# Kernel tuning notes

Measured on AMD Instinct MI355X. Metric: run time of the kernel, lower is better.

## Reference

```python
import jax, jax.numpy as jnp
import numpy as np

H = 32          # query heads
D = 128         # head_dim
THETA = 10000.0
NEG = -1e30


def _rope_cos_sin(positions, d):
    half = d // 2
    inv_freq = 1.0 / (THETA ** (jnp.arange(0, d, 2, dtype=jnp.float32) / d))  # [half]
    ang = positions.astype(jnp.float32)[:, None] * inv_freq[None, :]          # [B, half]
    return jnp.cos(ang), jnp.sin(ang)


def _apply_rope(x, cos, sin):
    # neox-style rotary on last dim; cos/sin broadcast over leading dims
    half = x.shape[-1] // 2
    x1, x2 = x[..., :half], x[..., half:]
    return jnp.concatenate([x1 * cos - x2 * sin, x2 * cos + x1 * sin], axis=-1)


def setup_inputs() -> dict:
    key = jax.random.key(0)
    ks = jax.random.split(key, 8)
    B, hidden = 64, 4096
    num_blocks, block_size, max_blocks = 16384, 16, 256
    hidden_states = jax.random.normal(ks[0], (B, hidden), dtype=jnp.float32)
    wqkv = jax.random.normal(ks[1], (hidden, (H + 2) * D), dtype=jnp.float32) * 0.02
    wdense = jax.random.normal(ks[2], (hidden, hidden), dtype=jnp.float32) * 0.02
    k_cache = jax.random.normal(ks[3], (num_blocks, block_size, D), dtype=jnp.float32)
    v_cache = jax.random.normal(ks[4], (num_blocks, block_size, D), dtype=jnp.float32)
    # each sequence owns a distinct set of 256 blocks
    block_tables = jnp.arange(B * max_blocks, dtype=jnp.int64).reshape(B, max_blocks)
    context_lens = jax.random.randint(ks[5], (B,), 1, max_blocks * block_size + 1).astype(jnp.int64)
    positions = context_lens - 1  # position of the new (current) token
    return {
        "hidden_states": hidden_states, "wqkv": wqkv, "wdense": wdense,
        "k_cache": k_cache, "v_cache": v_cache,
        "positions": positions, "block_tables": block_tables,
        "context_lens": context_lens,
    }


def reference(hidden_states, wqkv, wdense, k_cache, v_cache,
              positions, block_tables, context_lens):
    B = hidden_states.shape[0]
    block_size = k_cache.shape[1]
    scale = 1.0 / np.sqrt(D).astype(np.float32)

    # fused QKV projection (bias=False in Falcon-7B config)
    qkv = hidden_states @ wqkv                                  # [B,(H+2)*D]
    q = qkv[:, : H * D].reshape(B, H, D)
    k = qkv[:, H * D : (H + 1) * D]                             # [B,D]  (MQA, 1 kv head)
    v = qkv[:, (H + 1) * D :]                                   # [B,D]

    # rotary embedding on q and k at the current positions
    cos, sin = _rope_cos_sin(positions, D)                      # [B,D/2]
    q = _apply_rope(q, cos[:, None, :], sin[:, None, :])
    k = _apply_rope(k, cos, sin)

    # write the new token's k/v into the paged cache (scatter)
    rows = jnp.arange(B)
    blk = block_tables[rows, positions // block_size]           # [B]
    off = positions % block_size
    k_cache = k_cache.at[blk, off].set(k)
    v_cache = v_cache.at[blk, off].set(v)

    # paged gather: assemble each sequence's KV from its block table
    keys = k_cache[block_tables].reshape(B, -1, D)              # [B,L,D]
    vals = v_cache[block_tables].reshape(B, -1, D)
    L = keys.shape[1]

    scores = jnp.einsum('bhd,bld->bhl', q, keys) * scale        # [B,H,L]
    valid = jnp.arange(L)[None, :] < context_lens[:, None]      # [B,L]
    scores = jnp.where(valid[:, None, :], scores, NEG)
    probs = jax.nn.softmax(scores, axis=-1)
    attn = jnp.einsum('bhl,bld->bhd', probs, vals).reshape(B, H * D)

    return attn @ wdense                                        # [B,hidden]
```

## Files before the change

kernel.cpp:

```cpp
#include <hip/hip_runtime.h>
#include <hip/hip_bf16.h>
#include <cmath>

#define NHEADS 32
#define DIM 128
#define SPLITS 32
#define WIN 128
#define TILE 32
#define KSPLIT 16
#define QKV_N 4352
#define HID 4096

typedef __attribute__((ext_vector_type(4))) float f32x4;
typedef __attribute__((ext_vector_type(8))) short short8i;
typedef __attribute__((ext_vector_type(4))) short short4i;

__device__ __forceinline__ unsigned short f2bf(float x) {
  __hip_bfloat16 h = __float2bfloat16(x);
  return *reinterpret_cast<unsigned short*>(&h);
}
__device__ __forceinline__ unsigned int pk2bf(float lo, float hi) {
  return (unsigned)f2bf(lo) | ((unsigned)f2bf(hi) << 16);
}
__device__ __forceinline__ float bf2f(unsigned short u) {
  unsigned int b = ((unsigned int)u) << 16;
  return __uint_as_float(b);
}

__device__ __forceinline__ f32x4 mfma16bf16(short4i a, short4i b, f32x4 c) {
#if __has_builtin(__builtin_amdgcn_mfma_f32_16x16x16bf16_1k)
  return __builtin_amdgcn_mfma_f32_16x16x16bf16_1k(a, b, c, 0, 0, 0);
#else
  asm volatile("v_mfma_f32_16x16x16_bf16 %0, %1, %2, %0"
               : "+v"(c) : "v"(a), "v"(b));
  return c;
#endif
}

__global__ __launch_bounds__(256, 4) void gemm64_mfma(
    const float* __restrict__ A, const float* __restrict__ W,
    float* __restrict__ P, int N, int K)
{
  __shared__ unsigned short Ab[64][40];
  __shared__ unsigned short Wt[64][40];
  const int t = threadIdx.x;
  const int w = t >> 6, lane = t & 63;
  const int l4 = lane >> 4, l16 = lane & 15;
  const int n0 = blockIdx.x * 64;
  const int KS = K / KSPLIT;
  const int kbase = blockIdx.y * KS;

  const int ar = t >> 2, akq = t & 3;
  const int bn = t & 63, bkq = t >> 6;

  f32x4 acc[4];
#pragma unroll
  for (int i = 0; i < 4; ++i) acc[i] = (f32x4){0.f, 0.f, 0.f, 0.f};

  float4 a0, a1;
  float bw[8];

#define GLOAD(KC)                                                          \
  {                                                                        \
    const float* ap = A + (size_t)ar * K + kbase + (KC) + akq * 8;         \
    a0 = *(const float4*)ap;                                               \
    a1 = *(const float4*)(ap + 4);                                         \
    const float* wp = W + (size_t)(kbase + (KC) + bkq * 8) * N + n0 + bn;  \
    _Pragma("unroll")                                                      \
    for (int j = 0; j < 8; ++j) bw[j] = wp[(size_t)j * N];                 \
  }

#define SWRITE                                                             \
  {                                                                        \
    unsigned int ua[4] = {pk2bf(a0.x, a0.y), pk2bf(a0.z, a0.w),            \
                          pk2bf(a1.x, a1.y), pk2bf(a1.z, a1.w)};           \
    *(float4*)&Ab[ar][akq * 8] = *(float4*)ua;                             \
    unsigned int ub[4] = {pk2bf(bw[0], bw[1]), pk2bf(bw[2], bw[3]),        \
                          pk2bf(bw[4], bw[5]), pk2bf(bw[6], bw[7])};       \
    *(float4*)&Wt[bn][bkq * 8] = *(float4*)ub;                             \
  }

  GLOAD(0);
  SWRITE;
  __syncthreads();

  for (int kc = 0; kc < KS; kc += 32) {
    const bool pre = (kc + 32 < KS);
    if (pre) GLOAD(kc + 32);

    const short8i af = *(const short8i*)&Ab[w * 16 + l16][l4 * 8];
#pragma unroll
    for (int nt = 0; nt < 4; ++nt) {
      const short8i bf = *(const short8i*)&Wt[nt * 16 + l16][l4 * 8];
      acc[nt] = __builtin_amdgcn_mfma_f32_16x16x32_bf16(af, bf, acc[nt], 0, 0, 0);
    }

    __syncthreads();
    if (pre) {
      SWRITE;
      __syncthreads();
    }
  }

  float* base = P + (size_t)blockIdx.y * 64 * N + n0;
#pragma unroll
  for (int nt = 0; nt < 4; ++nt)
#pragma unroll
    for (int r = 0; r < 4; ++r)
      base[(size_t)(w * 16 + l4 * 4 + r) * N + nt * 16 + l16] = acc[nt][r];
#undef GLOAD
#undef SWRITE
}

__global__ __launch_bounds__(256) void reduce_parts(
    const float* __restrict__ P, float* __restrict__ C, int total)
{
  const int i = (blockIdx.x * 256 + threadIdx.x) * 4;
  if (i >= total) return;
  float4 s = *(const float4*)(P + i);
#pragma unroll
  for (int k = 1; k < KSPLIT; ++k) {
    const float4 v = *(const float4*)(P + (size_t)k * total + i);
    s.x += v.x; s.y += v.y; s.z += v.z; s.w += v.w;
  }
  *(float4*)(C + i) = s;
}

__global__ __launch_bounds__(256) void rope_kernel(
    float* __restrict__ qkv, const int* __restrict__ positions)
{
  const int b = blockIdx.x;
  float* row = qkv + (size_t)b * QKV_N;
  const float pos = (float)positions[b];
  for (int it = threadIdx.x; it < 33 * 64; it += 256) {
    const int r = it >> 6, i = it & 63;
    float* x = row + (r < 32 ? r * DIM : HID);
    const float ex = (float)(2 * i) * (1.0f / 128.0f);
    const float inv = 1.0f / powf(10000.0f, ex);
    const float ang = pos * inv;
    const float c = cosf(ang), sn = sinf(ang);
    const float x1 = x[i], x2 = x[i + 64];
    x[i]      = x1 * c - x2 * sn;
    x[i + 64] = x2 * c + x1 * sn;
  }
}

__global__ __launch_bounds__(256, 4) void attn_kernel(
    const float* __restrict__ qkv,
    const float* __restrict__ k_cache, const float* __restrict__ v_cache,
    const int* __restrict__ block_tables, const int* __restrict__ context_lens,
    float* __restrict__ pl, unsigned short* __restrict__ pacc)
{
  const int b = blockIdx.x, s = blockIdx.y;
  const int ctx = context_lens[b];
  const int start = s * WIN;
  if (start >= ctx) return;
  const int end = min(start + WIN, ctx);
  const int pos = ctx - 1;
  const int nt = (end - start + TILE - 1) / TILE;

  const int t = threadIdx.x;
  const int w = t >> 6, lane = t & 63;
  const int hq = w >> 1, pq = w & 1;
  const int l4 = lane >> 4, l16 = lane & 15;

  __shared__ unsigned short KbU[32 * 128];
  __shared__ unsigned short VtU[128 * 34];
  __shared__ float red[2][64][36];
  __shared__ int bt_lds[8];

  const float* qbase = qkv + (size_t)b * QKV_N;
  const int bt0 = start >> 4;
  if (t < 8) {
    const int idx = bt0 + t;
    bt_lds[t] = (idx < 256) ? block_tables[b * 256 + idx] : 0;
  }

  const float scale = 0.08838834764831845f;
  short8i qf[4];
  {
    const float* qp0 = qbase + (hq * 16 + l16) * DIM + l4 * 8;
#pragma unroll
    for (int ks = 0; ks < 4; ++ks) {
      const float4 a = *(const float4*)(qp0 + ks * 32);
      const float4 c = *(const float4*)(qp0 + ks * 32 + 4);
      union { unsigned int u[4]; short8i v; } qc;
      qc.u[0] = pk2bf(a.x * scale, a.y * scale);
      qc.u[1] = pk2bf(a.z * scale, a.w * scale);
      qc.u[2] = pk2bf(c.x * scale, c.y * scale);
      qc.u[3] = pk2bf(c.z * scale, c.w * scale);
      qf[ks] = qc.v;
    }
  }

  f32x4 o2[8];
#pragma unroll
  for (int i = 0; i < 8; ++i) o2[i] = (f32x4){0.f, 0.f, 0.f, 0.f};
  float lh = 0.f;

  float4 kreg[4], vreg[4];
  const int tk_sub = t >> 5;
  const int tk_col = t & 31;

#define LOADREGS(T0)                                                     \
  {                                                                      \
    _Pragma("unroll")                                                    \
    for (int j = 0; j < 4; ++j) {                                        \
      int gp_ = (T0) + j * 8 + tk_sub;                                   \
      if (gp_ > pos) gp_ = pos;                                          \
      const float* kp;                                                   \
      if (gp_ == pos) kp = qbase + HID;                                  \
      else {                                                             \
        const int blk = bt_lds[(gp_ >> 4) - bt0];                        \
        kp = k_cache + ((size_t)blk * 16 + (gp_ & 15)) * DIM;            \
      }                                                                  \
      kreg[j] = *(const float4*)(kp + tk_col * 4);                       \
    }                                                                    \
    int gv = (T0) + tk_col;                                              \
    if (gv > pos) gv = pos;                                              \
    const float* vp;                                                     \
    if (gv == pos) vp = qbase + HID + DIM;                               \
    else {                                                               \
      const int blk = bt_lds[(gv >> 4) - bt0];                           \
      vp = v_cache + ((size_t)blk * 16 + (gv & 15)) * DIM;               \
    }                                                                    \
    _Pragma("unroll")                                                    \
    for (int j = 0; j < 4; ++j)                                          \
      vreg[j] = *(const float4*)(vp + tk_sub * 16 + j * 4);              \
  }

#define WRITE_TILE                                                                     \
  {                                                                                    \
    _Pragma("unroll")                                                                  \
    for (int j = 0; j < 4; ++j) {                                                      \
      const int pl_ = j * 8 + tk_sub;                                                  \
      const int up = (tk_col >> 1) ^ (pl_ & 15);                                       \
      unsigned int lo = pk2bf(kreg[j].x, kreg[j].y);                                   \
      unsigned int hi = pk2bf(kreg[j].z, kreg[j].w);                                   \
      unsigned int* dst = (unsigned int*)&KbU[pl_ * 128 + up * 8 + (tk_col & 1) * 4];  \
      dst[0] = lo; dst[1] = hi;                                                        \
    }                                                                                  \
    _Pragma("unroll")                                                                  \
    for (int j = 0; j < 4; ++j) {                                                      \
      const int od0 = tk_sub * 16 + j * 4;                                             \
      VtU[(od0 + 0) * 34 + tk_col] = f2bf(vreg[j].x);                                  \
      VtU[(od0 + 1) * 34 + tk_col] = f2bf(vreg[j].y);                                  \
      VtU[(od0 + 2) * 34 + tk_col] = f2bf(vreg[j].z);                                  \
      VtU[(od0 + 3) * 34 + tk_col] = f2bf(vreg[j].w);                                  \
    }                                                                                  \
  }

  __syncthreads();
  LOADREGS(start);
  WRITE_TILE;
  __syncthreads();

  for (int it = 0; it < nt; ++it) {
    const int t0 = start + it * TILE;
    const bool pre = (it + 1 < nt);
    if (pre) LOADREGS(t0 + TILE);

    f32x4 accs = {0.f, 0.f, 0.f, 0.f};
    const int rowK = pq * 16 + l16;
#pragma unroll
    for (int ks = 0; ks < 4; ++ks) {
      const int up = (l4 + ks * 4) ^ l16;
      const short8i kf = *(const short8i*)&KbU[rowK * 128 + up * 8];
      accs = __builtin_amdgcn_mfma_f32_16x16x32_bf16(kf, qf[ks], accs, 0, 0, 0);
    }

    const int pb_ = t0 + pq * 16 + l4 * 4;
    const float p0 = (pb_ + 0 < end) ? __expf(accs[0]) : 0.f;
    const float p1 = (pb_ + 1 < end) ? __expf(accs[1]) : 0.f;
    const float p2 = (pb_ + 2 < end) ? __expf(accs[2]) : 0.f;
    const float p3 = (pb_ + 3 < end) ? __expf(accs[3]) : 0.f;
    lh += (p0 + p1) + (p2 + p3);
    union { unsigned int u[2]; short4i v; } pc;
    pc.u[0] = pk2bf(p0, p1);
    pc.u[1] = pk2bf(p2, p3);
    const short4i pf = pc.v;

    const int vb = pq * 16 + l4 * 4;
#pragma unroll
    for (int ob = 0; ob < 8; ++ob) {
      const int rowV = ob * 16 + l16;
      union { unsigned int u[2]; short4i v; } vc;
      vc.u[0] = *(const unsigned int*)&VtU[rowV * 34 + vb];
      vc.u[1] = *(const unsigned int*)&VtU[rowV * 34 + vb + 2];
      o2[ob] = mfma16bf16(pf, vc.v, o2[ob]);
    }

    if (pre) {
      __syncthreads();
      WRITE_TILE;
      __syncthreads();
    }
  }

  float lhr = lh;
  lhr += __shfl_xor(lhr, 16);
  lhr += __shfl_xor(lhr, 32);

  if (pq == 1) {
#pragma unroll
    for (int ob = 0; ob < 8; ++ob) *(f32x4*)&red[hq][lane][ob * 4] = o2[ob];
    red[hq][lane][32] = lhr;
  }
  __syncthreads();
  if (pq == 0) {
#pragma unroll
    for (int ob = 0; ob < 8; ++ob) {
      const f32x4 r4 = *(const f32x4*)&red[hq][lane][ob * 4];
      o2[ob] += r4;
    }
    lhr += red[hq][lane][32];
    const size_t sbase = (size_t)(b * SPLITS + s) * NHEADS + hq * 16;
#pragma unroll
    for (int ob = 0; ob < 8; ++ob) {
      pacc[(sbase + l4 * 4 + 0) * DIM + ob * 16 + l16] = f2bf(o2[ob][0]);
      pacc[(sbase + l4 * 4 + 1) * DIM + ob * 16 + l16] = f2bf(o2[ob][1]);
      pacc[(sbase + l4 * 4 + 2) * DIM + ob * 16 + l16] = f2bf(o2[ob][2]);
      pacc[(sbase + l4 * 4 + 3) * DIM + ob * 16 + l16] = f2bf(o2[ob][3]);
    }
    if (lane < 16) pl[sbase + lane] = lhr;
  }
#undef LOADREGS
#undef WRITE_TILE
}

__global__ __launch_bounds__(128) void combine_kernel(
    const float* __restrict__ pl, const unsigned short* __restrict__ pacc,
    const int* __restrict__ context_lens, float* __restrict__ attn)
{
  const int bh = blockIdx.x;
  const int b = bh >> 5, h = bh & 31;
  const int d = threadIdx.x;
  const int ctx = context_lens[b];
  const int ns = (ctx + WIN - 1) / WIN;
  float L = 0.f, o = 0.f;
  for (int s = 0; s < ns; ++s) {
    const size_t idx = (size_t)(b * SPLITS + s) * NHEADS + h;
    L += pl[idx];
    o += bf2f(pacc[idx * DIM + d]);
  }
  attn[(size_t)b * HID + h * DIM + d] = o / L;
}

extern "C" void kernel_launch(void* const* d_in, const int* in_sizes, int n_in,
                              void* d_out, int out_size, void* d_ws, size_t ws_size,
                              hipStream_t stream) {
  const float* hidden   = (const float*)d_in[0];
  const float* wqkv     = (const float*)d_in[1];
  const float* wdense   = (const float*)d_in[2];
  const float* k_cache  = (const float*)d_in[3];
  const float* v_cache  = (const float*)d_in[4];
  const int* positions    = (const int*)d_in[5];
  const int* block_tables = (const int*)d_in[6];
  const int* context_lens = (const int*)d_in[7];
  float* out = (float*)d_out;

  float* qkv  = (float*)d_ws;
  float* attn = qkv + 64 * QKV_N;
  float* un   = attn + 64 * HID;
  float* gp   = un;
  unsigned short* pacc = (unsigned short*)un;
  float* pl   = un + (size_t)64 * SPLITS * NHEADS * DIM / 2;

  gemm64_mfma<<<dim3(QKV_N / 64, KSPLIT), 256, 0, stream>>>(hidden, wqkv, gp, QKV_N, HID);
  reduce_parts<<<(64 * QKV_N) / 1024, 256, 0, stream>>>(gp, qkv, 64 * QKV_N);
  rope_kernel<<<64, 256, 0, stream>>>(qkv, positions);
  attn_kernel<<<dim3(64, SPLITS), 256, 0, stream>>>(qkv, k_cache, v_cache,
                                                    block_tables, context_lens, pl, pacc);
  combine_kernel<<<64 * NHEADS, 128, 0, stream>>>(pl, pacc, context_lens, attn);
  gemm64_mfma<<<dim3(HID / 64, KSPLIT), 256, 0, stream>>>(attn, wdense, gp, HID, HID);
  reduce_parts<<<(64 * HID) / 1024, 256, 0, stream>>>(gp, out, 64 * HID);
}
```

Baseline: 109.8 us.

## Balance attention splits by context length and drop intra-block head-pair reduction

Replaces fixed 128-token windows with per-sequence equal chunks across 16 splits, so every block does similar work. Each block now uses two waves (one per 16-head group) that cover all 32 tile rows themselves, removing the LDS reduction between wave pairs. V is stored row-major in LDS with both K and V loaded per token row. The combine kernel always sums all splits. Fewer threads per block and scalar 16-bit LDS reads for V fragments may reduce latency hiding and add LDS traffic.

```diff
diff --git a/kernel.cpp b/kernel.cpp
--- a/kernel.cpp
+++ b/kernel.cpp
@@ -4,12 +4,12 @@
 
 #define NHEADS 32
 #define DIM 128
-#define SPLITS 32
-#define WIN 128
+#define SPLITS 16
 #define TILE 32
 #define KSPLIT 16
 #define QKV_N 4352
 #define HID 4096
+#define VSTR 132
 
 typedef __attribute__((ext_vector_type(4))) float f32x4;
 typedef __attribute__((ext_vector_type(8))) short short8i;
@@ -145,37 +145,35 @@
   }
 }
 
-__global__ __launch_bounds__(256, 4) void attn_kernel(
+__global__ __launch_bounds__(128, 3) void attn_kernel(
     const float* __restrict__ qkv,
     const float* __restrict__ k_cache, const float* __restrict__ v_cache,
     const int* __restrict__ block_tables, const int* __restrict__ context_lens,
     float* __restrict__ pl, unsigned short* __restrict__ pacc)
 {
   const int b = blockIdx.x, s = blockIdx.y;
-  const int ctx = context_lens[b];
-  const int start = s * WIN;
-  if (start >= ctx) return;
-  const int end = min(start + WIN, ctx);
-  const int pos = ctx - 1;
-  const int nt = (end - start + TILE - 1) / TILE;
-
   const int t = threadIdx.x;
   const int w = t >> 6, lane = t & 63;
-  const int hq = w >> 1, pq = w & 1;
   const int l4 = lane >> 4, l16 = lane & 15;
+  const int ctx = context_lens[b];
+  const int pos = ctx - 1;
+  const int chunk = (ctx + SPLITS - 1) / SPLITS;
+  const int start = s * chunk;
+  const int end = min(start + chunk, ctx);
+  const int nt = (end > start) ? ((end - start + TILE - 1) / TILE) : 0;
 
   __shared__ unsigned short KbU[32 * 128];
-  __shared__ unsigned short VtU[128 * 34];
-  __shared__ float red[2][64][36];
-  __shared__ int bt_lds[8];
+  __shared__ unsigned short VL[TILE][VSTR];
+  __shared__ int bt_lds[20];
 
   const float* qbase = qkv + (size_t)b * QKV_N;
   const int bt0 = start >> 4;
-  if (t < 8) {
+  if (t < 20) {
     const int idx = bt0 + t;
     bt_lds[t] = (idx < 256) ? block_tables[b * 256 + idx] : 0;
   }
 
+  const int hq = w;
   const float scale = 0.08838834764831845f;
   short8i qf[4];
   {
@@ -198,102 +196,94 @@
   for (int i = 0; i < 8; ++i) o2[i] = (f32x4){0.f, 0.f, 0.f, 0.f};
   float lh = 0.f;
 
-  float4 kreg[4], vreg[4];
-  const int tk_sub = t >> 5;
-  const int tk_col = t & 31;
+  const int tcol = t & 31;
+  const int tsub = t >> 5;
+  float4 kreg[8], vreg[8];
 
 #define LOADREGS(T0)                                                     \
   {                                                                      \
     _Pragma("unroll")                                                    \
-    for (int j = 0; j < 4; ++j) {                                        \
-      int gp_ = (T0) + j * 8 + tk_sub;                                   \
+    for (int j = 0; j < 8; ++j) {                                        \
+      int gp_ = (T0) + j * 4 + tsub;                                     \
       if (gp_ > pos) gp_ = pos;                                          \
-      const float* kp;                                                   \
-      if (gp_ == pos) kp = qbase + HID;                                  \
+      const float *kp, *vp;                                              \
+      if (gp_ == pos) { kp = qbase + HID; vp = qbase + HID + DIM; }      \
       else {                                                             \
         const int blk = bt_lds[(gp_ >> 4) - bt0];                        \
-        kp = k_cache + ((size_t)blk * 16 + (gp_ & 15)) * DIM;            \
+        const size_t cidx = ((size_t)blk * 16 + (gp_ & 15)) * DIM;       \
+        kp = k_cache + cidx; vp = v_cache + cidx;                        \
       }                                                                  \
-      kreg[j] = *(const float4*)(kp + tk_col * 4);                       \
+      kreg[j] = ((const float4*)kp)[tcol];                               \
+      vreg[j] = ((const float4*)vp)[tcol];                               \
     }                                                                    \
-    int gv = (T0) + tk_col;                                              \
-    if (gv > pos) gv = pos;                                              \
-    const float* vp;                                                     \
-    if (gv == pos) vp = qbase + HID + DIM;                               \
-    else {                                                               \
-      const int blk = bt_lds[(gv >> 4) - bt0];                           \
-      vp = v_cache + ((size_t)blk * 16 + (gv & 15)) * DIM;               \
-    }                                                                    \
-    _Pragma("unroll")                                                    \
-    for (int j = 0; j < 4; ++j)                                          \
-      vreg[j] = *(const float4*)(vp + tk_sub * 16 + j * 4);              \
-  }
-
-#define WRITE_TILE                                                                     \
-  {                                                                                    \
-    _Pragma("unroll")                                                                  \
-    for (int j = 0; j < 4; ++j) {                                                      \
-      const int pl_ = j * 8 + tk_sub;                                                  \
-      const int up = (tk_col >> 1) ^ (pl_ & 15);                                       \
-      unsigned int lo = pk2bf(kreg[j].x, kreg[j].y);                                   \
-      unsigned int hi = pk2bf(kreg[j].z, kreg[j].w);                                   \
-      unsigned int* dst = (unsigned int*)&KbU[pl_ * 128 + up * 8 + (tk_col & 1) * 4];  \
-      dst[0] = lo; dst[1] = hi;                                                        \
-    }                                                                                  \
-    _Pragma("unroll")                                                                  \
-    for (int j = 0; j < 4; ++j) {                                                      \
-      const int od0 = tk_sub * 16 + j * 4;                                             \
-      VtU[(od0 + 0) * 34 + tk_col] = f2bf(vreg[j].x);                                  \
-      VtU[(od0 + 1) * 34 + tk_col] = f2bf(vreg[j].y);                                  \
-      VtU[(od0 + 2) * 34 + tk_col] = f2bf(vreg[j].z);                                  \
-      VtU[(od0 + 3) * 34 + tk_col] = f2bf(vreg[j].w);                                  \
-    }                                                                                  \
-  }
-
-  __syncthreads();
-  LOADREGS(start);
-  WRITE_TILE;
-  __syncthreads();
-
-  for (int it = 0; it < nt; ++it) {
-    const int t0 = start + it * TILE;
-    const bool pre = (it + 1 < nt);
-    if (pre) LOADREGS(t0 + TILE);
-
-    f32x4 accs = {0.f, 0.f, 0.f, 0.f};
-    const int rowK = pq * 16 + l16;
-#pragma unroll
-    for (int ks = 0; ks < 4; ++ks) {
-      const int up = (l4 + ks * 4) ^ l16;
-      const short8i kf = *(const short8i*)&KbU[rowK * 128 + up * 8];
-      accs = __builtin_amdgcn_mfma_f32_16x16x32_bf16(kf, qf[ks], accs, 0, 0, 0);
-    }
-
-    const int pb_ = t0 + pq * 16 + l4 * 4;
-    const float p0 = (pb_ + 0 < end) ? __expf(accs[0]) : 0.f;
-    const float p1 = (pb_ + 1 < end) ? __expf(accs[1]) : 0.f;
-    const float p2 = (pb_ + 2 < end) ? __expf(accs[2]) : 0.f;
-    const float p3 = (pb_ + 3 < end) ? __expf(accs[3]) : 0.f;
-    lh += (p0 + p1) + (p2 + p3);
-    union { unsigned int u[2]; short4i v; } pc;
-    pc.u[0] = pk2bf(p0, p1);
-    pc.u[1] = pk2bf(p2, p3);
-    const short4i pf = pc.v;
-
-    const int vb = pq * 16 + l4 * 4;
-#pragma unroll
-    for (int ob = 0; ob < 8; ++ob) {
-      const int rowV = ob * 16 + l16;
-      union { unsigned int u[2]; short4i v; } vc;
-      vc.u[0] = *(const unsigned int*)&VtU[rowV * 34 + vb];
-      vc.u[1] = *(const unsigned int*)&VtU[rowV * 34 + vb + 2];
-      o2[ob] = mfma16bf16(pf, vc.v, o2[ob]);
-    }
-
-    if (pre) {
-      __syncthreads();
-      WRITE_TILE;
-      __syncthreads();
+  }
+
+#define WRITE_TILE                                                                  \
+  {                                                                                 \
+    _Pragma("unroll")                                                               \
+    for (int j = 0; j < 8; ++j) {                                                   \
+      const int row = j * 4 + tsub;                                                 \
+      const int up = (tcol >> 1) ^ (row & 15);                                      \
+      unsigned int* kd = (unsigned int*)&KbU[row * 128 + up * 8 + (tcol & 1) * 4];  \
+      kd[0] = pk2bf(kreg[j].x, kreg[j].y);                                          \
+      kd[1] = pk2bf(kreg[j].z, kreg[j].w);                                          \
+      unsigned int* vd = (unsigned int*)&VL[row][tcol * 4];                         \
+      vd[0] = pk2bf(vreg[j].x, vreg[j].y);                                          \
+      vd[1] = pk2bf(vreg[j].z, vreg[j].w);                                          \
+    }                                                                               \
+  }
+
+  if (nt > 0) {
+    __syncthreads();
+    LOADREGS(start);
+    WRITE_TILE;
+    __syncthreads();
+
+    for (int it = 0; it < nt; ++it) {
+      const int t0 = start + it * TILE;
+      const bool pre = (it + 1 < nt);
+      if (pre) LOADREGS(t0 + TILE);
+
+      short4i pf[2];
+#pragma unroll
+      for (int pg = 0; pg < 2; ++pg) {
+        f32x4 accs = {0.f, 0.f, 0.f, 0.f};
+        const int rowK = pg * 16 + l16;
+#pragma unroll
+        for (int ks = 0; ks < 4; ++ks) {
+          const int up = (l4 + ks * 4) ^ l16;
+          const short8i kf = *(const short8i*)&KbU[rowK * 128 + up * 8];
+          accs = __builtin_amdgcn_mfma_f32_16x16x32_bf16(kf, qf[ks], accs, 0, 0, 0);
+        }
+        const int pb_ = t0 + pg * 16 + l4 * 4;
+        const float p0 = (pb_ + 0 < end) ? __expf(accs[0]) : 0.f;
+        const float p1 = (pb_ + 1 < end) ? __expf(accs[1]) : 0.f;
+        const float p2 = (pb_ + 2 < end) ? __expf(accs[2]) : 0.f;
+        const float p3 = (pb_ + 3 < end) ? __expf(accs[3]) : 0.f;
+        lh += (p0 + p1) + (p2 + p3);
+        union { unsigned int u[2]; short4i v; } pc;
+        pc.u[0] = pk2bf(p0, p1);
+        pc.u[1] = pk2bf(p2, p3);
+        pf[pg] = pc.v;
+      }
+
+#pragma unroll
+      for (int ob = 0; ob < 8; ++ob) {
+#pragma unroll
+        for (int pg = 0; pg < 2; ++pg) {
+          union { unsigned short su[4]; short4i v; } vc;
+#pragma unroll
+          for (int j = 0; j < 4; ++j)
+            vc.su[j] = VL[pg * 16 + l4 * 4 + j][ob * 16 + l16];
+          o2[ob] = mfma16bf16(pf[pg], vc.v, o2[ob]);
+        }
+      }
+
+      if (pre) {
+        __syncthreads();
+        WRITE_TILE;
+        __syncthreads();
+      }
     }
   }
 
@@ -301,44 +291,29 @@
   lhr += __shfl_xor(lhr, 16);
   lhr += __shfl_xor(lhr, 32);
 
-  if (pq == 1) {
-#pragma unroll
-    for (int ob = 0; ob < 8; ++ob) *(f32x4*)&red[hq][lane][ob * 4] = o2[ob];
-    red[hq][lane][32] = lhr;
-  }
-  __syncthreads();
-  if (pq == 0) {
-#pragma unroll
-    for (int ob = 0; ob < 8; ++ob) {
-      const f32x4 r4 = *(const f32x4*)&red[hq][lane][ob * 4];
-      o2[ob] += r4;
-    }
-    lhr += red[hq][lane][32];
-    const size_t sbase = (size_t)(b * SPLITS + s) * NHEADS + hq * 16;
-#pragma unroll
-    for (int ob = 0; ob < 8; ++ob) {
-      pacc[(sbase + l4 * 4 + 0) * DIM + ob * 16 + l16] = f2bf(o2[ob][0]);
-      pacc[(sbase + l4 * 4 + 1) * DIM + ob * 16 + l16] = f2bf(o2[ob][1]);
-      pacc[(sbase + l4 * 4 + 2) * DIM + ob * 16 + l16] = f2bf(o2[ob][2]);
-      pacc[(sbase + l4 * 4 + 3) * DIM + ob * 16 + l16] = f2bf(o2[ob][3]);
-    }
-    if (lane < 16) pl[sbase + lane] = lhr;
-  }
+  const size_t sbase = (size_t)(b * SPLITS + s) * NHEADS + hq * 16;
+#pragma unroll
+  for (int ob = 0; ob < 8; ++ob) {
+    pacc[(sbase + l4 * 4 + 0) * DIM + ob * 16 + l16] = f2bf(o2[ob][0]);
+    pacc[(sbase + l4 * 4 + 1) * DIM + ob * 16 + l16] = f2bf(o2[ob][1]);
+    pacc[(sbase + l4 * 4 + 2) * DIM + ob * 16 + l16] = f2bf(o2[ob][2]);
+    pacc[(sbase + l4 * 4 + 3) * DIM + ob * 16 + l16] = f2bf(o2[ob][3]);
+  }
+  if (lane < 16) pl[sbase + lane] = lhr;
 #undef LOADREGS
 #undef WRITE_TILE
 }
 
 __global__ __launch_bounds__(128) void combine_kernel(
     const float* __restrict__ pl, const unsigned short* __restrict__ pacc,
-    const int* __restrict__ context_lens, float* __restrict__ attn)
+    float* __restrict__ attn)
 {
   const int bh = blockIdx.x;
   const int b = bh >> 5, h = bh & 31;
   const int d = threadIdx.x;
-  const int ctx = context_lens[b];
-  const int ns = (ctx + WIN - 1) / WIN;
   float L = 0.f, o = 0.f;
-  for (int s = 0; s < ns; ++s) {
+#pragma unroll
+  for (int s = 0; s < SPLITS; ++s) {
     const size_t idx = (size_t)(b * SPLITS + s) * NHEADS + h;
     L += pl[idx];
     o += bf2f(pacc[idx * DIM + d]);
@@ -369,9 +344,9 @@
   gemm64_mfma<<<dim3(QKV_N / 64, KSPLIT), 256, 0, stream>>>(hidden, wqkv, gp, QKV_N, HID);
   reduce_parts<<<(64 * QKV_N) / 1024, 256, 0, stream>>>(gp, qkv, 64 * QKV_N);
   rope_kernel<<<64, 256, 0, stream>>>(qkv, positions);
-  attn_kernel<<<dim3(64, SPLITS), 256, 0, stream>>>(qkv, k_cache, v_cache,
+  attn_kernel<<<dim3(64, SPLITS), 128, 0, stream>>>(qkv, k_cache, v_cache,
                                                     block_tables, context_lens, pl, pacc);
-  combine_kernel<<<64 * NHEADS, 128, 0, stream>>>(pl, pacc, context_lens, attn);
+  combine_kernel<<<64 * NHEADS, 128, 0, stream>>>(pl, pacc, attn);
   gemm64_mfma<<<dim3(HID / 64, KSPLIT), 256, 0, stream>>>(attn, wdense, gp, HID, HID);
   reduce_parts<<<(64 * HID) / 1024, 256, 0, stream>>>(gp, out, 64 * HID);
 }
```

Measured after the change: 206.7 us. +88.2%, slower.

## Balance attention splits per sequence, double-buffer LDS tiles, drop in-block reduction

Applied to the files above, without the earlier changes.

Replaces fixed 128-token windows with a per-sequence chunk of ctx/16 tokens, so every one of the 16 split blocks per sequence gets equal work instead of short sequences leaving blocks idle and long ones serialized. K/V tiles are double-buffered in LDS, cutting one barrier per iteration and overlapping the next tile's stores with compute. The cross-wave LDS reduction is removed: each half-wave pair writes its own partial, and the combine kernel always sums 32 partials. This brings larger LDS use, which may lower occupancy, more partial-buffer traffic, and empty splits that write zero partials.

```diff
diff --git a/kernel.cpp b/kernel.cpp
--- a/kernel.cpp
+++ b/kernel.cpp
@@ -4,12 +4,12 @@
 
 #define NHEADS 32
 #define DIM 128
-#define SPLITS 32
-#define WIN 128
+#define SPLITS 16
 #define TILE 32
 #define KSPLIT 16
 #define QKV_N 4352
 #define HID 4096
+#define VSTR 36
 
 typedef __attribute__((ext_vector_type(4))) float f32x4;
 typedef __attribute__((ext_vector_type(8))) short short8i;
@@ -152,26 +152,24 @@
     float* __restrict__ pl, unsigned short* __restrict__ pacc)
 {
   const int b = blockIdx.x, s = blockIdx.y;
-  const int ctx = context_lens[b];
-  const int start = s * WIN;
-  if (start >= ctx) return;
-  const int end = min(start + WIN, ctx);
-  const int pos = ctx - 1;
-  const int nt = (end - start + TILE - 1) / TILE;
-
   const int t = threadIdx.x;
   const int w = t >> 6, lane = t & 63;
   const int hq = w >> 1, pq = w & 1;
   const int l4 = lane >> 4, l16 = lane & 15;
-
-  __shared__ unsigned short KbU[32 * 128];
-  __shared__ unsigned short VtU[128 * 34];
-  __shared__ float red[2][64][36];
-  __shared__ int bt_lds[8];
+  const int ctx = context_lens[b];
+  const int pos = ctx - 1;
+  const int chunk = (ctx + SPLITS - 1) / SPLITS;
+  const int start = s * chunk;
+  const int end = min(start + chunk, ctx);
+  const int nt = (end > start) ? ((end - start + TILE - 1) / TILE) : 0;
+
+  __shared__ unsigned short KbU[2][32 * 128];
+  __shared__ unsigned short VtU[2][128 * VSTR];
+  __shared__ int bt_lds[20];
 
   const float* qbase = qkv + (size_t)b * QKV_N;
   const int bt0 = start >> 4;
-  if (t < 8) {
+  if (t < 20) {
     const int idx = bt0 + t;
     bt_lds[t] = (idx < 256) ? block_tables[b * 256 + idx] : 0;
   }
@@ -229,71 +227,68 @@
       vreg[j] = *(const float4*)(vp + tk_sub * 16 + j * 4);              \
   }
 
-#define WRITE_TILE                                                                     \
+#define WRITE_TILE(BUF)                                                                \
   {                                                                                    \
     _Pragma("unroll")                                                                  \
     for (int j = 0; j < 4; ++j) {                                                      \
       const int pl_ = j * 8 + tk_sub;                                                  \
       const int up = (tk_col >> 1) ^ (pl_ & 15);                                       \
-      unsigned int lo = pk2bf(kreg[j].x, kreg[j].y);                                   \
-      unsigned int hi = pk2bf(kreg[j].z, kreg[j].w);                                   \
-      unsigned int* dst = (unsigned int*)&KbU[pl_ * 128 + up * 8 + (tk_col & 1) * 4];  \
-      dst[0] = lo; dst[1] = hi;                                                        \
+      unsigned int* kd =                                                               \
+          (unsigned int*)&KbU[BUF][pl_ * 128 + up * 8 + (tk_col & 1) * 4];             \
+      kd[0] = pk2bf(kreg[j].x, kreg[j].y);                                             \
+      kd[1] = pk2bf(kreg[j].z, kreg[j].w);                                             \
     }                                                                                  \
     _Pragma("unroll")                                                                  \
     for (int j = 0; j < 4; ++j) {                                                      \
       const int od0 = tk_sub * 16 + j * 4;                                             \
-      VtU[(od0 + 0) * 34 + tk_col] = f2bf(vreg[j].x);                                  \
-      VtU[(od0 + 1) * 34 + tk_col] = f2bf(vreg[j].y);                                  \
-      VtU[(od0 + 2) * 34 + tk_col] = f2bf(vreg[j].z);                                  \
-      VtU[(od0 + 3) * 34 + tk_col] = f2bf(vreg[j].w);                                  \
+      VtU[BUF][(od0 + 0) * VSTR + tk_col] = f2bf(vreg[j].x);                           \
+      VtU[BUF][(od0 + 1) * VSTR + tk_col] = f2bf(vreg[j].y);                           \
+      VtU[BUF][(od0 + 2) * VSTR + tk_col] = f2bf(vreg[j].z);                           \
+      VtU[BUF][(od0 + 3) * VSTR + tk_col] = f2bf(vreg[j].w);                           \
     }                                                                                  \
   }
 
-  __syncthreads();
-  LOADREGS(start);
-  WRITE_TILE;
-  __syncthreads();
-
-  for (int it = 0; it < nt; ++it) {
-    const int t0 = start + it * TILE;
-    const bool pre = (it + 1 < nt);
-    if (pre) LOADREGS(t0 + TILE);
-
-    f32x4 accs = {0.f, 0.f, 0.f, 0.f};
-    const int rowK = pq * 16 + l16;
-#pragma unroll
-    for (int ks = 0; ks < 4; ++ks) {
-      const int up = (l4 + ks * 4) ^ l16;
-      const short8i kf = *(const short8i*)&KbU[rowK * 128 + up * 8];
-      accs = __builtin_amdgcn_mfma_f32_16x16x32_bf16(kf, qf[ks], accs, 0, 0, 0);
-    }
-
-    const int pb_ = t0 + pq * 16 + l4 * 4;
-    const float p0 = (pb_ + 0 < end) ? __expf(accs[0]) : 0.f;
-    const float p1 = (pb_ + 1 < end) ? __expf(accs[1]) : 0.f;
-    const float p2 = (pb_ + 2 < end) ? __expf(accs[2]) : 0.f;
-    const float p3 = (pb_ + 3 < end) ? __expf(accs[3]) : 0.f;
-    lh += (p0 + p1) + (p2 + p3);
-    union { unsigned int u[2]; short4i v; } pc;
-    pc.u[0] = pk2bf(p0, p1);
-    pc.u[1] = pk2bf(p2, p3);
-    const short4i pf = pc.v;
-
-    const int vb = pq * 16 + l4 * 4;
-#pragma unroll
-    for (int ob = 0; ob < 8; ++ob) {
-      const int rowV = ob * 16 + l16;
-      union { unsigned int u[2]; short4i v; } vc;
-      vc.u[0] = *(const unsigned int*)&VtU[rowV * 34 + vb];
-      vc.u[1] = *(const unsigned int*)&VtU[rowV * 34 + vb + 2];
-      o2[ob] = mfma16bf16(pf, vc.v, o2[ob]);
-    }
-
-    if (pre) {
+  if (nt > 0) {
+    __syncthreads();
+    LOADREGS(start);
+    WRITE_TILE(0);
+
+    for (int it = 0; it < nt; ++it) {
+      const int t0 = start + it * TILE;
+      const int cur = it & 1;
+      const bool pre = (it + 1 < nt);
+      if (pre) LOADREGS(t0 + TILE);
       __syncthreads();
-      WRITE_TILE;
-      __syncthreads();
+
+      f32x4 accs = {0.f, 0.f, 0.f, 0.f};
+      const int rowK = pq * 16 + l16;
+#pragma unroll
+      for (int ks = 0; ks < 4; ++ks) {
+        const int up = (l4 + ks * 4) ^ l16;
+        const short8i kf = *(const short8i*)&KbU[cur][rowK * 128 + up * 8];
+        accs = __builtin_amdgcn_mfma_f32_16x16x32_bf16(kf, qf[ks], accs, 0, 0, 0);
+      }
+
+      const int pb_ = t0 + pq * 16 + l4 * 4;
+      const float p0 = (pb_ + 0 < end) ? __expf(accs[0]) : 0.f;
+      const float p1 = (pb_ + 1 < end) ? __expf(accs[1]) : 0.f;
+      const float p2 = (pb_ + 2 < end) ? __expf(accs[2]) : 0.f;
+      const float p3 = (pb_ + 3 < end) ? __expf(accs[3]) : 0.f;
+      lh += (p0 + p1) + (p2 + p3);
+      union { unsigned int u[2]; short4i v; } pc;
+      pc.u[0] = pk2bf(p0, p1);
+      pc.u[1] = pk2bf(p2, p3);
+      const short4i pf = pc.v;
+
+      const int vb = pq * 16 + l4 * 4;
+#pragma unroll
+      for (int ob = 0; ob < 8; ++ob) {
+        const short4i vv =
+            *(const short4i*)&VtU[cur][(ob * 16 + l16) * VSTR + vb];
+        o2[ob] = mfma16bf16(pf, vv, o2[ob]);
+      }
+
+      if (pre) WRITE_TILE(cur ^ 1);
     }
   }
 
@@ -301,45 +296,30 @@
   lhr += __shfl_xor(lhr, 16);
   lhr += __shfl_xor(lhr, 32);
 
-  if (pq == 1) {
-#pragma unroll
-    for (int ob = 0; ob < 8; ++ob) *(f32x4*)&red[hq][lane][ob * 4] = o2[ob];
-    red[hq][lane][32] = lhr;
-  }
-  __syncthreads();
-  if (pq == 0) {
-#pragma unroll
-    for (int ob = 0; ob < 8; ++ob) {
-      const f32x4 r4 = *(const f32x4*)&red[hq][lane][ob * 4];
-      o2[ob] += r4;
-    }
-    lhr += red[hq][lane][32];
-    const size_t sbase = (size_t)(b * SPLITS + s) * NHEADS + hq * 16;
-#pragma unroll
-    for (int ob = 0; ob < 8; ++ob) {
-      pacc[(sbase + l4 * 4 + 0) * DIM + ob * 16 + l16] = f2bf(o2[ob][0]);
-      pacc[(sbase + l4 * 4 + 1) * DIM + ob * 16 + l16] = f2bf(o2[ob][1]);
-      pacc[(sbase + l4 * 4 + 2) * DIM + ob * 16 + l16] = f2bf(o2[ob][2]);
-      pacc[(sbase + l4 * 4 + 3) * DIM + ob * 16 + l16] = f2bf(o2[ob][3]);
-    }
-    if (lane < 16) pl[sbase + lane] = lhr;
-  }
+  const size_t slot = ((size_t)(b * SPLITS + s) * 2 + pq) * NHEADS + hq * 16;
+#pragma unroll
+  for (int ob = 0; ob < 8; ++ob) {
+    pacc[(slot + l4 * 4 + 0) * DIM + ob * 16 + l16] = f2bf(o2[ob][0]);
+    pacc[(slot + l4 * 4 + 1) * DIM + ob * 16 + l16] = f2bf(o2[ob][1]);
+    pacc[(slot + l4 * 4 + 2) * DIM + ob * 16 + l16] = f2bf(o2[ob][2]);
+    pacc[(slot + l4 * 4 + 3) * DIM + ob * 16 + l16] = f2bf(o2[ob][3]);
+  }
+  if (lane < 16) pl[slot + lane] = lhr;
 #undef LOADREGS
 #undef WRITE_TILE
 }
 
 __global__ __launch_bounds__(128) void combine_kernel(
     const float* __restrict__ pl, const unsigned short* __restrict__ pacc,
-    const int* __restrict__ context_lens, float* __restrict__ attn)
+    float* __restrict__ attn)
 {
   const int bh = blockIdx.x;
   const int b = bh >> 5, h = bh & 31;
   const int d = threadIdx.x;
-  const int ctx = context_lens[b];
-  const int ns = (ctx + WIN - 1) / WIN;
   float L = 0.f, o = 0.f;
-  for (int s = 0; s < ns; ++s) {
-    const size_t idx = (size_t)(b * SPLITS + s) * NHEADS + h;
+#pragma unroll 4
+  for (int j = 0; j < SPLITS * 2; ++j) {
+    const size_t idx = ((size_t)b * SPLITS * 2 + j) * NHEADS + h;
     L += pl[idx];
     o += bf2f(pacc[idx * DIM + d]);
   }
@@ -364,14 +344,14 @@
   float* un   = attn + 64 * HID;
   float* gp   = un;
   unsigned short* pacc = (unsigned short*)un;
-  float* pl   = un + (size_t)64 * SPLITS * NHEADS * DIM / 2;
+  float* pl   = un + (size_t)64 * SPLITS * 2 * NHEADS * DIM / 2;
 
   gemm64_mfma<<<dim3(QKV_N / 64, KSPLIT), 256, 0, stream>>>(hidden, wqkv, gp, QKV_N, HID);
   reduce_parts<<<(64 * QKV_N) / 1024, 256, 0, stream>>>(gp, qkv, 64 * QKV_N);
   rope_kernel<<<64, 256, 0, stream>>>(qkv, positions);
   attn_kernel<<<dim3(64, SPLITS), 256, 0, stream>>>(qkv, k_cache, v_cache,
                                                     block_tables, context_lens, pl, pacc);
-  combine_kernel<<<64 * NHEADS, 128, 0, stream>>>(pl, pacc, context_lens, attn);
+  combine_kernel<<<64 * NHEADS, 128, 0, stream>>>(pl, pacc, attn);
   gemm64_mfma<<<dim3(HID / 64, KSPLIT), 256, 0, stream>>>(attn, wdense, gp, HID, HID);
   reduce_parts<<<(64 * HID) / 1024, 256, 0, stream>>>(gp, out, 64 * HID);
 }
```

Result: no change. 109.2 us (-0.5%).
